# Optimization experiments

Measured on AMD Instinct MI355X. Metric: run time of the kernel, lower is better.

Reference implementation:

```python
import jax, jax.numpy as jnp
import numpy as np

N_NODES = 50000
N_EDGES = 800000
IN_FEATS = 128
HID = 64
HEADS = 3
NUM_CLASSES = 8
ATTN_SLOPE = 0.2   # DGL GATConv leaky_relu slope on attention logits
ACT_SLOPE = 0.01   # nn.LeakyReLU default


def setup_inputs() -> dict:
    key = jax.random.key(0)
    ks = jax.random.split(key, 40)
    inp = {}
    inp["x"] = jax.random.normal(ks[0], (N_NODES, IN_FEATS), dtype=jnp.float32)
    inp["src"] = jax.random.randint(ks[1], (N_EDGES,), 0, N_NODES)
    inp["dst"] = jax.random.randint(ks[2], (N_EDGES,), 0, N_NODES)
    dims_in = [IN_FEATS, HID, HID, HID, HID]
    i = 3
    for l, din in enumerate(dims_in, start=1):
        inp[f"W{l}"] = jax.random.normal(ks[i], (din, HEADS * HID), dtype=jnp.float32) / np.float32(np.sqrt(din)); i += 1
        inp[f"b{l}"] = jnp.zeros((HEADS * HID,), dtype=jnp.float32)
        inp[f"al{l}"] = jax.random.normal(ks[i], (HEADS, HID), dtype=jnp.float32) * 0.1; i += 1
        inp[f"ar{l}"] = jax.random.normal(ks[i], (HEADS, HID), dtype=jnp.float32) * 0.1; i += 1
    inp["Wo"] = jax.random.normal(ks[i], (HID, NUM_CLASSES), dtype=jnp.float32) / np.float32(np.sqrt(HID)); i += 1
    inp["bo"] = jnp.zeros((NUM_CLASSES,), dtype=jnp.float32)
    return inp


def _gatconv(h, W, b, al, ar, src, dst):
    # h: [N, din] -> feat: [N, H, F]
    feat = (h @ W).reshape(N_NODES, HEADS, HID)
    el = jnp.einsum('nhf,hf->nh', feat, al)   # [N, H]
    er = jnp.einsum('nhf,hf->nh', feat, ar)   # [N, H]
    e = jax.nn.leaky_relu(el[src] + er[dst], ATTN_SLOPE)        # [E, H]
    # numerically-stable edge softmax segmented by destination node
    m = jax.ops.segment_max(e, dst, num_segments=N_NODES)      # [N, H]
    ex = jnp.exp(e - m[dst])                                   # [E, H]
    denom = jax.ops.segment_sum(ex, dst, num_segments=N_NODES)  # [N, H]
    alpha = ex / denom[dst]                                    # [E, H]
    msg = alpha[:, :, None] * feat[src]                        # [E, H, F]
    out = jax.ops.segment_sum(msg, dst, num_segments=N_NODES)  # [N, H, F]
    return out + b.reshape(HEADS, HID)


def reference(x, src, dst,
              W1, b1, al1, ar1,
              W2, b2, al2, ar2,
              W3, b3, al3, ar3,
              W4, b4, al4, ar4,
              W5, b5, al5, ar5,
              Wo, bo):
    layers = [(W1, b1, al1, ar1), (W2, b2, al2, ar2), (W3, b3, al3, ar3),
              (W4, b4, al4, ar4), (W5, b5, al5, ar5)]
    h = x
    for (W, b, al, ar) in layers:
        h = jax.nn.leaky_relu(_gatconv(h, W, b, al, ar, src, dst), ACT_SLOPE)
        h = h.mean(axis=1)  # mean over heads -> [N, F]
    return h @ Wo + bo      # [N, num_classes]
```

## Files before the change

kernel.cpp:

```cpp
#include <hip/hip_runtime.h>
#include <hip/hip_fp16.h>
#include <cstdint>

#define N_NODES 50000
#define N_EDGES 800000
#define IN_FEATS 128
#define HID 64
#define HEADS 3
#define NUM_CLASSES 8
#define ATTN_SLOPE 0.2f
#define ACT_SLOPE 0.01f

__device__ __forceinline__ float lrelu(float x, float s) { return x > 0.f ? x : s * x; }

__global__ void k_deg(const int* __restrict__ dst, int* __restrict__ deg, int E) {
    int i = blockIdx.x * blockDim.x + threadIdx.x;
    if (i < E) atomicAdd(&deg[dst[i]], 1);
}

__global__ __launch_bounds__(256) void k_scan1(const int* __restrict__ deg, int* __restrict__ off,
                                               int* __restrict__ bsum, int n) {
    __shared__ int wtot[4];
    int tid = threadIdx.x;
    int lane = tid & 63, wid = tid >> 6;
    int base = blockIdx.x * 2048 + tid * 8;
    int v[8];
    if (base + 8 <= n) {
        int4 a = *(const int4*)&deg[base];
        int4 b = *(const int4*)&deg[base + 4];
        v[0] = a.x; v[1] = a.y; v[2] = a.z; v[3] = a.w;
        v[4] = b.x; v[5] = b.y; v[6] = b.z; v[7] = b.w;
    } else {
#pragma unroll
        for (int j = 0; j < 8; ++j) v[j] = (base + j < n) ? deg[base + j] : 0;
    }
    int s[8];
    s[0] = v[0];
#pragma unroll
    for (int j = 1; j < 8; ++j) s[j] = s[j - 1] + v[j];
    int t = s[7];
    int incl = t;
    for (int o = 1; o < 64; o <<= 1) {
        int u = __shfl_up(incl, o);
        if (lane >= o) incl += u;
    }
    int excl = incl - t;
    if (lane == 63) wtot[wid] = incl;
    __syncthreads();
    int wprefix = 0;
    for (int w = 0; w < wid; ++w) wprefix += wtot[w];
    int base_off = wprefix + excl;
#pragma unroll
    for (int j = 0; j < 8; ++j)
        if (base + j < n) off[base + j] = base_off + s[j] - v[j];
    if (tid == 0) bsum[blockIdx.x] = wtot[0] + wtot[1] + wtot[2] + wtot[3];
}

__global__ __launch_bounds__(64) void k_scan2(int* __restrict__ bsum, int nb) {
    int tid = threadIdx.x;
    int v = (tid < nb) ? bsum[tid] : 0;
    int incl = v;
    for (int o = 1; o < 64; o <<= 1) {
        int u = __shfl_up(incl, o);
        if (tid >= o) incl += u;
    }
    if (tid < nb) bsum[tid] = incl - v;
}

__global__ __launch_bounds__(256) void k_scan3(int* __restrict__ off, const int* __restrict__ bsum,
                                               int n, int E) {
    int i = blockIdx.x * blockDim.x + threadIdx.x;
    if (i < n) off[i] += bsum[i >> 11];
    if (i == 0) off[n] = E;
}

__global__ void k_fill(const int* __restrict__ src, const int* __restrict__ dst,
                       const int* __restrict__ off, int* __restrict__ cur,
                       int* __restrict__ ssrc, int E) {
    int i = blockIdx.x * blockDim.x + threadIdx.x;
    if (i < E) {
        int d = dst[i];
        int p = atomicAdd(&cur[d], 1);
        ssrc[off[d] + p] = src[i];
    }
}

__global__ __launch_bounds__(256) void k_gemm(const float* __restrict__ h, const float* __restrict__ W,
                                              const float* __restrict__ al, const float* __restrict__ ar,
                                              __half* __restrict__ feat,
                                              float* __restrict__ el, float* __restrict__ er,
                                              int N, int din) {
    __shared__ float Hl[128][68];
    __shared__ float Wl[64][64];
    int tid = threadIdx.x;
    int cg = tid & 15;
    int rg = tid >> 4;
    int row0 = blockIdx.x * 128;
    int head = blockIdx.y;
    int c0 = head * 64;

    float acc[8][4];
#pragma unroll
    for (int i = 0; i < 8; ++i)
#pragma unroll
        for (int c = 0; c < 4; ++c) acc[i][c] = 0.f;

    for (int k0 = 0; k0 < din; k0 += 64) {
        for (int j = tid; j < 1024; j += 256) {
            int k = j >> 4, c4 = (j & 15) << 2;
            *(float4*)&Wl[k][c4] = *(const float4*)&W[(size_t)(k0 + k) * 192 + c0 + c4];
        }
        for (int j = tid; j < 2048; j += 256) {
            int r = j >> 4, kk = (j & 15) << 2;
            int row = row0 + r;
            float4 v = make_float4(0.f, 0.f, 0.f, 0.f);
            if (row < N) v = *(const float4*)&h[(size_t)row * din + k0 + kk];
            *(float4*)&Hl[r][kk] = v;
        }
        __syncthreads();

        for (int k = 0; k < 64; k += 4) {
            float4 w0 = *(const float4*)&Wl[k + 0][cg << 2];
            float4 w1 = *(const float4*)&Wl[k + 1][cg << 2];
            float4 w2 = *(const float4*)&Wl[k + 2][cg << 2];
            float4 w3 = *(const float4*)&Wl[k + 3][cg << 2];
#pragma unroll
            for (int i = 0; i < 8; ++i) {
                float4 hv = *(const float4*)&Hl[rg + 16 * i][k];
                acc[i][0] += hv.x * w0.x + hv.y * w1.x + hv.z * w2.x + hv.w * w3.x;
                acc[i][1] += hv.x * w0.y + hv.y * w1.y + hv.z * w2.y + hv.w * w3.y;
                acc[i][2] += hv.x * w0.z + hv.y * w1.z + hv.z * w2.z + hv.w * w3.z;
                acc[i][3] += hv.x * w0.w + hv.y * w1.w + hv.z * w2.w + hv.w * w3.w;
            }
        }
        __syncthreads();
    }

    float alv0 = al[c0 + (cg << 2) + 0], alv1 = al[c0 + (cg << 2) + 1];
    float alv2 = al[c0 + (cg << 2) + 2], alv3 = al[c0 + (cg << 2) + 3];
    float arv0 = ar[c0 + (cg << 2) + 0], arv1 = ar[c0 + (cg << 2) + 1];
    float arv2 = ar[c0 + (cg << 2) + 2], arv3 = ar[c0 + (cg << 2) + 3];
#pragma unroll
    for (int i = 0; i < 8; ++i) {
        int row = row0 + rg + 16 * i;
        bool ok = (row < N);
        float4 a4 = make_float4(acc[i][0], acc[i][1], acc[i][2], acc[i][3]);
        if (ok) {
            union { __half2 h2[2]; uint2 u; } pk;
            pk.h2[0] = __floats2half2_rn(a4.x, a4.y);
            pk.h2[1] = __floats2half2_rn(a4.z, a4.w);
            *(uint2*)&feat[(size_t)row * 192 + c0 + (cg << 2)] = pk.u;
        }
        float pl = a4.x * alv0 + a4.y * alv1 + a4.z * alv2 + a4.w * alv3;
        float pr = a4.x * arv0 + a4.y * arv1 + a4.z * arv2 + a4.w * arv3;
        for (int o = 1; o < 16; o <<= 1) {
            pl += __shfl_xor(pl, o);
            pr += __shfl_xor(pr, o);
        }
        if (ok && cg == 0) {
            el[row * HEADS + head] = pl;
            er[row * HEADS + head] = pr;
        }
    }
}

__global__ __launch_bounds__(256) void k_agg(const int* __restrict__ off, const int* __restrict__ ssrc,
                                             const float* __restrict__ el, const float* __restrict__ er,
                                             const __half* __restrict__ feat, const float* __restrict__ b,
                                             float* __restrict__ hout, int N) {
    __shared__ float4 ebuf[4][64];
    int wib = threadIdx.x >> 6;
    int wid = (blockIdx.x * blockDim.x + threadIdx.x) >> 6;
    int lane = threadIdx.x & 63;
    if (wid >= N) return;
    int start = off[wid], end = off[wid + 1];
    int cnt = end - start;
    float er0 = er[wid * HEADS + 0];
    float er1 = er[wid * HEADS + 1];
    float er2 = er[wid * HEADS + 2];
    float acc0 = 0.f, acc1 = 0.f, acc2 = 0.f;
    float den0 = 0.f, den1 = 0.f, den2 = 0.f;

    if (cnt <= 64) {
        int s0 = 0;
        float ea = -3.4e38f, eb = -3.4e38f, ec = -3.4e38f;
        if (lane < cnt) {
            s0 = ssrc[start + lane];
            ea = lrelu(el[s0 * HEADS + 0] + er0, ATTN_SLOPE);
            eb = lrelu(el[s0 * HEADS + 1] + er1, ATTN_SLOPE);
            ec = lrelu(el[s0 * HEADS + 2] + er2, ATTN_SLOPE);
        }
        float ma = ea, mb = eb, mc = ec;
        for (int o = 32; o > 0; o >>= 1) {
            ma = fmaxf(ma, __shfl_xor(ma, o));
            mb = fmaxf(mb, __shfl_xor(mb, o));
            mc = fmaxf(mc, __shfl_xor(mc, o));
        }
        float xa = (lane < cnt) ? __expf(ea - ma) : 0.f;
        float xb = (lane < cnt) ? __expf(eb - mb) : 0.f;
        float xc = (lane < cnt) ? __expf(ec - mc) : 0.f;
        float da = xa, db = xb, dc = xc;
        for (int o = 32; o > 0; o >>= 1) {
            da += __shfl_xor(da, o);
            db += __shfl_xor(db, o);
            dc += __shfl_xor(dc, o);
        }
        den0 = da; den1 = db; den2 = dc;
        ebuf[wib][lane] = make_float4(__int_as_float(s0), xa, xb, xc);
        int t = 0;
        for (; t + 4 <= cnt; t += 4) {
            float4 v0 = ebuf[wib][t + 0];
            float4 v1 = ebuf[wib][t + 1];
            float4 v2 = ebuf[wib][t + 2];
            float4 v3 = ebuf[wib][t + 3];
            const __half* f0 = feat + (size_t)__float_as_int(v0.x) * 192 + lane;
            const __half* f1 = feat + (size_t)__float_as_int(v1.x) * 192 + lane;
            const __half* f2 = feat + (size_t)__float_as_int(v2.x) * 192 + lane;
            const __half* f3 = feat + (size_t)__float_as_int(v3.x) * 192 + lane;
            float p00 = __half2float(f0[0]), p01 = __half2float(f0[64]), p02 = __half2float(f0[128]);
            float p10 = __half2float(f1[0]), p11 = __half2float(f1[64]), p12 = __half2float(f1[128]);
            float p20 = __half2float(f2[0]), p21 = __half2float(f2[64]), p22 = __half2float(f2[128]);
            float p30 = __half2float(f3[0]), p31 = __half2float(f3[64]), p32 = __half2float(f3[128]);
            acc0 += v0.y * p00; acc1 += v0.z * p01; acc2 += v0.w * p02;
            acc0 += v1.y * p10; acc1 += v1.z * p11; acc2 += v1.w * p12;
            acc0 += v2.y * p20; acc1 += v2.z * p21; acc2 += v2.w * p22;
            acc0 += v3.y * p30; acc1 += v3.z * p31; acc2 += v3.w * p32;
        }
        for (; t < cnt; ++t) {
            float4 v = ebuf[wib][t];
            const __half* fr = feat + (size_t)__float_as_int(v.x) * 192 + lane;
            acc0 += v.y * __half2float(fr[0]);
            acc1 += v.z * __half2float(fr[64]);
            acc2 += v.w * __half2float(fr[128]);
        }
    } else {
        float ma = -3.4e38f, mb = -3.4e38f, mc = -3.4e38f;
        for (int j = start + lane; j < end; j += 64) {
            int s = ssrc[j];
            ma = fmaxf(ma, lrelu(el[s * HEADS + 0] + er0, ATTN_SLOPE));
            mb = fmaxf(mb, lrelu(el[s * HEADS + 1] + er1, ATTN_SLOPE));
            mc = fmaxf(mc, lrelu(el[s * HEADS + 2] + er2, ATTN_SLOPE));
        }
        for (int o = 32; o > 0; o >>= 1) {
            ma = fmaxf(ma, __shfl_xor(ma, o));
            mb = fmaxf(mb, __shfl_xor(mb, o));
            mc = fmaxf(mc, __shfl_xor(mc, o));
        }
        float da = 0.f, db = 0.f, dc = 0.f;
        for (int j0 = start; j0 < end; j0 += 64) {
            int jj = j0 + lane;
            int s0 = 0;
            float xa = 0.f, xb = 0.f, xc = 0.f;
            if (jj < end) {
                s0 = ssrc[jj];
                xa = __expf(lrelu(el[s0 * HEADS + 0] + er0, ATTN_SLOPE) - ma);
                xb = __expf(lrelu(el[s0 * HEADS + 1] + er1, ATTN_SLOPE) - mb);
                xc = __expf(lrelu(el[s0 * HEADS + 2] + er2, ATTN_SLOPE) - mc);
            }
            da += xa; db += xb; dc += xc;
            ebuf[wib][lane] = make_float4(__int_as_float(s0), xa, xb, xc);
            int c = min(64, end - j0);
            int t = 0;
            for (; t + 4 <= c; t += 4) {
                float4 v0 = ebuf[wib][t + 0];
                float4 v1 = ebuf[wib][t + 1];
                float4 v2 = ebuf[wib][t + 2];
                float4 v3 = ebuf[wib][t + 3];
                const __half* f0 = feat + (size_t)__float_as_int(v0.x) * 192 + lane;
                const __half* f1 = feat + (size_t)__float_as_int(v1.x) * 192 + lane;
                const __half* f2 = feat + (size_t)__float_as_int(v2.x) * 192 + lane;
                const __half* f3 = feat + (size_t)__float_as_int(v3.x) * 192 + lane;
                float p00 = __half2float(f0[0]), p01 = __half2float(f0[64]), p02 = __half2float(f0[128]);
                float p10 = __half2float(f1[0]), p11 = __half2float(f1[64]), p12 = __half2float(f1[128]);
                float p20 = __half2float(f2[0]), p21 = __half2float(f2[64]), p22 = __half2float(f2[128]);
                float p30 = __half2float(f3[0]), p31 = __half2float(f3[64]), p32 = __half2float(f3[128]);
                acc0 += v0.y * p00; acc1 += v0.z * p01; acc2 += v0.w * p02;
                acc0 += v1.y * p10; acc1 += v1.z * p11; acc2 += v1.w * p12;
                acc0 += v2.y * p20; acc1 += v2.z * p21; acc2 += v2.w * p22;
                acc0 += v3.y * p30; acc1 += v3.z * p31; acc2 += v3.w * p32;
            }
            for (; t < c; ++t) {
                float4 v = ebuf[wib][t];
                const __half* fr = feat + (size_t)__float_as_int(v.x) * 192 + lane;
                acc0 += v.y * __half2float(fr[0]);
                acc1 += v.z * __half2float(fr[64]);
                acc2 += v.w * __half2float(fr[128]);
            }
        }
        for (int o = 32; o > 0; o >>= 1) {
            da += __shfl_xor(da, o);
            db += __shfl_xor(db, o);
            dc += __shfl_xor(dc, o);
        }
        den0 = da; den1 = db; den2 = dc;
    }

    float v0 = (cnt > 0) ? acc0 / den0 : 0.f;
    float v1 = (cnt > 0) ? acc1 / den1 : 0.f;
    float v2 = (cnt > 0) ? acc2 / den2 : 0.f;
    float hsum = lrelu(v0 + b[lane], ACT_SLOPE)
               + lrelu(v1 + b[64 + lane], ACT_SLOPE)
               + lrelu(v2 + b[128 + lane], ACT_SLOPE);
    hout[wid * 64 + lane] = hsum * (1.f / 3.f);
}

__global__ __launch_bounds__(256) void k_out(const float* __restrict__ h, const float* __restrict__ Wo,
                                             const float* __restrict__ bo, float* __restrict__ out, int N) {
    __shared__ float Hl[32][65];
    __shared__ float Wl[64 * 8];
    int tid = threadIdx.x;
    int n0 = blockIdx.x * 32;
    for (int i = tid; i < 32 * 64; i += 256) {
        int r = i >> 6, k = i & 63;
        Hl[r][k] = (n0 + r < N) ? h[(n0 + r) * 64 + k] : 0.f;
    }
    for (int i = tid; i < 512; i += 256) Wl[i] = Wo[i];
    __syncthreads();
    int r = tid >> 3, c = tid & 7;
    float acc = 0.f;
    for (int k = 0; k < 64; ++k) acc += Hl[r][k] * Wl[k * 8 + c];
    int row = n0 + r;
    if (row < N) out[row * 8 + c] = acc + bo[c];
}

extern "C" void kernel_launch(void* const* d_in, const int* in_sizes, int n_in,
                              void* d_out, int out_size, void* d_ws, size_t ws_size,
                              hipStream_t stream) {
    const float* x  = (const float*)d_in[0];
    const int* src  = (const int*)d_in[1];
    const int* dst  = (const int*)d_in[2];
    const float *W[5], *b[5], *al[5], *ar[5];
    for (int l = 0; l < 5; ++l) {
        W[l]  = (const float*)d_in[3 + l * 4];
        b[l]  = (const float*)d_in[4 + l * 4];
        al[l] = (const float*)d_in[5 + l * 4];
        ar[l] = (const float*)d_in[6 + l * 4];
    }
    const float* Wo = (const float*)d_in[23];
    const float* bo = (const float*)d_in[24];
    float* out = (float*)d_out;

    char* ws = (char*)d_ws;
    auto alloc = [&](size_t bytes) {
        char* p = ws;
        ws += (bytes + 255) & ~size_t(255);
        return p;
    };
    __half* feat = (__half*)alloc(sizeof(__half) * (size_t)N_NODES * 192);
    float* el   = (float*)alloc(sizeof(float) * (size_t)N_NODES * HEADS);
    float* er   = (float*)alloc(sizeof(float) * (size_t)N_NODES * HEADS);
    float* h0   = (float*)alloc(sizeof(float) * (size_t)N_NODES * 64);
    float* h1   = (float*)alloc(sizeof(float) * (size_t)N_NODES * 64);
    int* deg    = (int*)alloc(sizeof(int) * N_NODES);
    int* off    = (int*)alloc(sizeof(int) * (N_NODES + 1));
    int* cur    = (int*)alloc(sizeof(int) * N_NODES);
    int* ssrc   = (int*)alloc(sizeof(int) * N_EDGES);
    int* bsum   = (int*)alloc(sizeof(int) * 64);

    const int NB = (N_NODES + 2047) / 2048;
    hipMemsetAsync(deg, 0, sizeof(int) * N_NODES, stream);
    hipMemsetAsync(cur, 0, sizeof(int) * N_NODES, stream);
    k_deg<<<(N_EDGES + 255) / 256, 256, 0, stream>>>(dst, deg, N_EDGES);
    k_scan1<<<NB, 256, 0, stream>>>(deg, off, bsum, N_NODES);
    k_scan2<<<1, 64, 0, stream>>>(bsum, NB);
    k_scan3<<<(N_NODES + 255) / 256, 256, 0, stream>>>(off, bsum, N_NODES, N_EDGES);
    k_fill<<<(N_EDGES + 255) / 256, 256, 0, stream>>>(src, dst, off, cur, ssrc, N_EDGES);

    const float* hin = x;
    float* hbuf[2] = {h0, h1};
    int din = IN_FEATS;
    for (int l = 0; l < 5; ++l) {
        dim3 ggrid((N_NODES + 127) / 128, HEADS);
        k_gemm<<<ggrid, 256, 0, stream>>>(hin, W[l], al[l], ar[l], feat, el, er, N_NODES, din);
        float* hn = hbuf[l & 1];
        k_agg<<<(N_NODES * 64 + 255) / 256, 256, 0, stream>>>(off, ssrc, el, er, feat, b[l], hn, N_NODES);
        hin = hn;
        din = HID;
    }
    k_out<<<(N_NODES + 31) / 32, 256, 0, stream>>>(hin, Wo, bo, out, N_NODES);
}
```

Baseline: 624.1 us.

## Use fp16 MFMA for per-layer GEMM and store hidden activations in fp16

Replaces the fp32 scalar-FMA GEMM with MFMA 16x16x32 fp16 instructions. The input x and the weights are pre-cast to fp16 (weights transposed) in two new kernels. Hidden activations between layers are now stored as fp16, which halves GEMM input bandwidth. In exchange it adds two cast kernels, uses uncoalesced scalar half stores for feat in the epilogue, and lowers precision of the activations.

```diff
diff --git a/kernel.cpp b/kernel.cpp
--- a/kernel.cpp
+++ b/kernel.cpp
@@ -10,6 +10,9 @@
 #define NUM_CLASSES 8
 #define ATTN_SLOPE 0.2f
 #define ACT_SLOPE 0.01f
+
+typedef _Float16 half8 __attribute__((ext_vector_type(8)));
+typedef float f32x4 __attribute__((ext_vector_type(4)));
 
 __device__ __forceinline__ float lrelu(float x, float s) { return x > 0.f ? x : s * x; }
 
@@ -85,81 +88,118 @@
     }
 }
 
-__global__ __launch_bounds__(256) void k_gemm(const float* __restrict__ h, const float* __restrict__ W,
+__global__ __launch_bounds__(256) void k_xcast(const float* __restrict__ x, _Float16* __restrict__ xh, int n8) {
+    int i = blockIdx.x * blockDim.x + threadIdx.x;
+    if (i < n8) {
+        float4 a = *(const float4*)&x[i * 8];
+        float4 b = *(const float4*)&x[i * 8 + 4];
+        _Float16 v[8] = {(_Float16)a.x, (_Float16)a.y, (_Float16)a.z, (_Float16)a.w,
+                         (_Float16)b.x, (_Float16)b.y, (_Float16)b.z, (_Float16)b.w};
+        *(uint4*)&xh[i * 8] = *(uint4*)v;
+    }
+}
+
+__global__ __launch_bounds__(256) void k_wcast(const float* __restrict__ W1, const float* __restrict__ W2,
+                                               const float* __restrict__ W3, const float* __restrict__ W4,
+                                               const float* __restrict__ W5, _Float16* __restrict__ Wt) {
+    int i = blockIdx.x * blockDim.x + threadIdx.x;
+    if (i >= 24576 + 4 * 12288) return;
+    const float* W; int din; int idx; _Float16* out;
+    if (i < 24576) { W = W1; din = 128; idx = i; out = Wt; }
+    else {
+        int j = i - 24576; int l = j / 12288; idx = j % 12288;
+        W = (l == 0) ? W2 : (l == 1) ? W3 : (l == 2) ? W4 : W5;
+        din = 64;
+        out = Wt + 24576 + l * 12288;
+    }
+    int col = idx / din, k = idx % din;
+    out[idx] = (_Float16)W[k * 192 + col];
+}
+
+__global__ __launch_bounds__(256) void k_gemm(const _Float16* __restrict__ h, const _Float16* __restrict__ Wt,
                                               const float* __restrict__ al, const float* __restrict__ ar,
-                                              __half* __restrict__ feat,
+                                              _Float16* __restrict__ feat,
                                               float* __restrict__ el, float* __restrict__ er,
                                               int N, int din) {
-    __shared__ float Hl[128][68];
-    __shared__ float Wl[64][64];
+    __shared__ __align__(16) _Float16 Hl[128 * 136];
+    __shared__ __align__(16) _Float16 Wl[64 * 136];
+    const int K = din;
+    const int LD = K + 8;
+    const int KC = K >> 3;
     int tid = threadIdx.x;
-    int cg = tid & 15;
-    int rg = tid >> 4;
     int row0 = blockIdx.x * 128;
     int head = blockIdx.y;
     int c0 = head * 64;
 
-    float acc[8][4];
-#pragma unroll
-    for (int i = 0; i < 8; ++i)
-#pragma unroll
-        for (int c = 0; c < 4; ++c) acc[i][c] = 0.f;
-
-    for (int k0 = 0; k0 < din; k0 += 64) {
-        for (int j = tid; j < 1024; j += 256) {
-            int k = j >> 4, c4 = (j & 15) << 2;
-            *(float4*)&Wl[k][c4] = *(const float4*)&W[(size_t)(k0 + k) * 192 + c0 + c4];
-        }
-        for (int j = tid; j < 2048; j += 256) {
-            int r = j >> 4, kk = (j & 15) << 2;
-            int row = row0 + r;
-            float4 v = make_float4(0.f, 0.f, 0.f, 0.f);
-            if (row < N) v = *(const float4*)&h[(size_t)row * din + k0 + kk];
-            *(float4*)&Hl[r][kk] = v;
-        }
-        __syncthreads();
-
-        for (int k = 0; k < 64; k += 4) {
-            float4 w0 = *(const float4*)&Wl[k + 0][cg << 2];
-            float4 w1 = *(const float4*)&Wl[k + 1][cg << 2];
-            float4 w2 = *(const float4*)&Wl[k + 2][cg << 2];
-            float4 w3 = *(const float4*)&Wl[k + 3][cg << 2];
-#pragma unroll
-            for (int i = 0; i < 8; ++i) {
-                float4 hv = *(const float4*)&Hl[rg + 16 * i][k];
-                acc[i][0] += hv.x * w0.x + hv.y * w1.x + hv.z * w2.x + hv.w * w3.x;
-                acc[i][1] += hv.x * w0.y + hv.y * w1.y + hv.z * w2.y + hv.w * w3.y;
-                acc[i][2] += hv.x * w0.z + hv.y * w1.z + hv.z * w2.z + hv.w * w3.z;
-                acc[i][3] += hv.x * w0.w + hv.y * w1.w + hv.z * w2.w + hv.w * w3.w;
-            }
-        }
-        __syncthreads();
-    }
-
-    float alv0 = al[c0 + (cg << 2) + 0], alv1 = al[c0 + (cg << 2) + 1];
-    float alv2 = al[c0 + (cg << 2) + 2], alv3 = al[c0 + (cg << 2) + 3];
-    float arv0 = ar[c0 + (cg << 2) + 0], arv1 = ar[c0 + (cg << 2) + 1];
-    float arv2 = ar[c0 + (cg << 2) + 2], arv3 = ar[c0 + (cg << 2) + 3];
-#pragma unroll
-    for (int i = 0; i < 8; ++i) {
-        int row = row0 + rg + 16 * i;
-        bool ok = (row < N);
-        float4 a4 = make_float4(acc[i][0], acc[i][1], acc[i][2], acc[i][3]);
-        if (ok) {
-            union { __half2 h2[2]; uint2 u; } pk;
-            pk.h2[0] = __floats2half2_rn(a4.x, a4.y);
-            pk.h2[1] = __floats2half2_rn(a4.z, a4.w);
-            *(uint2*)&feat[(size_t)row * 192 + c0 + (cg << 2)] = pk.u;
-        }
-        float pl = a4.x * alv0 + a4.y * alv1 + a4.z * alv2 + a4.w * alv3;
-        float pr = a4.x * arv0 + a4.y * arv1 + a4.z * arv2 + a4.w * arv3;
-        for (int o = 1; o < 16; o <<= 1) {
-            pl += __shfl_xor(pl, o);
-            pr += __shfl_xor(pr, o);
-        }
-        if (ok && cg == 0) {
-            el[row * HEADS + head] = pl;
-            er[row * HEADS + head] = pr;
+    for (int i = tid; i < 64 * KC; i += 256) {
+        int col = i / KC, c8 = i % KC;
+        *(uint4*)&Wl[col * LD + c8 * 8] = *(const uint4*)&Wt[(size_t)(c0 + col) * K + c8 * 8];
+    }
+    for (int i = tid; i < 128 * KC; i += 256) {
+        int r = i / KC, c8 = i % KC;
+        int row = row0 + r;
+        uint4 v = make_uint4(0, 0, 0, 0);
+        if (row < N) v = *(const uint4*)&h[(size_t)row * K + c8 * 8];
+        *(uint4*)&Hl[r * LD + c8 * 8] = v;
+    }
+    __syncthreads();
+
+    int wid = tid >> 6, lane = tid & 63;
+    int l15 = lane & 15;
+    int koff = (lane >> 4) * 8;
+    int wr0 = wid * 32;
+
+    f32x4 acc[2][4] = {};
+    int nkb = K >> 5;
+    for (int kb = 0; kb < nkb; ++kb) {
+        int kbase = kb * 32 + koff;
+        half8 a0 = *(half8*)&Hl[(wr0 + l15) * LD + kbase];
+        half8 a1 = *(half8*)&Hl[(wr0 + 16 + l15) * LD + kbase];
+        half8 b0 = *(half8*)&Wl[(l15) * LD + kbase];
+        half8 b1 = *(half8*)&Wl[(16 + l15) * LD + kbase];
+        half8 b2 = *(half8*)&Wl[(32 + l15) * LD + kbase];
+        half8 b3 = *(half8*)&Wl[(48 + l15) * LD + kbase];
+        acc[0][0] = __builtin_amdgcn_mfma_f32_16x16x32_f16(a0, b0, acc[0][0], 0, 0, 0);
+        acc[0][1] = __builtin_amdgcn_mfma_f32_16x16x32_f16(a0, b1, acc[0][1], 0, 0, 0);
+        acc[0][2] = __builtin_amdgcn_mfma_f32_16x16x32_f16(a0, b2, acc[0][2], 0, 0, 0);
+        acc[0][3] = __builtin_amdgcn_mfma_f32_16x16x32_f16(a0, b3, acc[0][3], 0, 0, 0);
+        acc[1][0] = __builtin_amdgcn_mfma_f32_16x16x32_f16(a1, b0, acc[1][0], 0, 0, 0);
+        acc[1][1] = __builtin_amdgcn_mfma_f32_16x16x32_f16(a1, b1, acc[1][1], 0, 0, 0);
+        acc[1][2] = __builtin_amdgcn_mfma_f32_16x16x32_f16(a1, b2, acc[1][2], 0, 0, 0);
+        acc[1][3] = __builtin_amdgcn_mfma_f32_16x16x32_f16(a1, b3, acc[1][3], 0, 0, 0);
+    }
+
+    float alv[4], arv[4];
+#pragma unroll
+    for (int ct = 0; ct < 4; ++ct) {
+        alv[ct] = al[c0 + ct * 16 + l15];
+        arv[ct] = ar[c0 + ct * 16 + l15];
+    }
+
+#pragma unroll
+    for (int rt = 0; rt < 2; ++rt) {
+#pragma unroll
+        for (int r = 0; r < 4; ++r) {
+            int row = row0 + wr0 + rt * 16 + (lane >> 4) * 4 + r;
+            bool ok = (row < N);
+            float c0v = acc[rt][0][r], c1v = acc[rt][1][r], c2v = acc[rt][2][r], c3v = acc[rt][3][r];
+            if (ok) {
+                size_t base = (size_t)row * 192 + c0;
+                feat[base + l15]      = (_Float16)c0v;
+                feat[base + 16 + l15] = (_Float16)c1v;
+                feat[base + 32 + l15] = (_Float16)c2v;
+                feat[base + 48 + l15] = (_Float16)c3v;
+            }
+            float pl = c0v * alv[0] + c1v * alv[1] + c2v * alv[2] + c3v * alv[3];
+            float pr = c0v * arv[0] + c1v * arv[1] + c2v * arv[2] + c3v * arv[3];
+            for (int o = 1; o < 16; o <<= 1) {
+                pl += __shfl_xor(pl, o);
+                pr += __shfl_xor(pr, o);
+            }
+            if (ok && l15 == 0) {
+                el[row * HEADS + head] = pl;
+                er[row * HEADS + head] = pr;
+            }
         }
     }
 }
@@ -167,7 +207,7 @@
 __global__ __launch_bounds__(256) void k_agg(const int* __restrict__ off, const int* __restrict__ ssrc,
                                              const float* __restrict__ el, const float* __restrict__ er,
                                              const __half* __restrict__ feat, const float* __restrict__ b,
-                                             float* __restrict__ hout, int N) {
+                                             __half* __restrict__ hout, int N) {
     __shared__ float4 ebuf[4][64];
     int wib = threadIdx.x >> 6;
     int wid = (blockIdx.x * blockDim.x + threadIdx.x) >> 6;
@@ -301,10 +341,10 @@
     float hsum = lrelu(v0 + b[lane], ACT_SLOPE)
                + lrelu(v1 + b[64 + lane], ACT_SLOPE)
                + lrelu(v2 + b[128 + lane], ACT_SLOPE);
-    hout[wid * 64 + lane] = hsum * (1.f / 3.f);
-}
-
-__global__ __launch_bounds__(256) void k_out(const float* __restrict__ h, const float* __restrict__ Wo,
+    hout[wid * 64 + lane] = __float2half(hsum * (1.f / 3.f));
+}
+
+__global__ __launch_bounds__(256) void k_out(const __half* __restrict__ h, const float* __restrict__ Wo,
                                              const float* __restrict__ bo, float* __restrict__ out, int N) {
     __shared__ float Hl[32][65];
     __shared__ float Wl[64 * 8];
@@ -312,7 +352,7 @@
     int n0 = blockIdx.x * 32;
     for (int i = tid; i < 32 * 64; i += 256) {
         int r = i >> 6, k = i & 63;
-        Hl[r][k] = (n0 + r < N) ? h[(n0 + r) * 64 + k] : 0.f;
+        Hl[r][k] = (n0 + r < N) ? __half2float(h[(n0 + r) * 64 + k]) : 0.f;
     }
     for (int i = tid; i < 512; i += 256) Wl[i] = Wo[i];
     __syncthreads();
@@ -346,11 +386,13 @@
         ws += (bytes + 255) & ~size_t(255);
         return p;
     };
-    __half* feat = (__half*)alloc(sizeof(__half) * (size_t)N_NODES * 192);
-    float* el   = (float*)alloc(sizeof(float) * (size_t)N_NODES * HEADS);
-    float* er   = (float*)alloc(sizeof(float) * (size_t)N_NODES * HEADS);
-    float* h0   = (float*)alloc(sizeof(float) * (size_t)N_NODES * 64);
-    float* h1   = (float*)alloc(sizeof(float) * (size_t)N_NODES * 64);
+    _Float16* feat = (_Float16*)alloc(sizeof(_Float16) * (size_t)N_NODES * 192);
+    float* el      = (float*)alloc(sizeof(float) * (size_t)N_NODES * HEADS);
+    float* er      = (float*)alloc(sizeof(float) * (size_t)N_NODES * HEADS);
+    _Float16* xh   = (_Float16*)alloc(sizeof(_Float16) * (size_t)N_NODES * IN_FEATS);
+    _Float16* h0   = (_Float16*)alloc(sizeof(_Float16) * (size_t)N_NODES * 64);
+    _Float16* h1   = (_Float16*)alloc(sizeof(_Float16) * (size_t)N_NODES * 64);
+    _Float16* wt   = (_Float16*)alloc(sizeof(_Float16) * (24576 + 4 * 12288));
     int* deg    = (int*)alloc(sizeof(int) * N_NODES);
     int* off    = (int*)alloc(sizeof(int) * (N_NODES + 1));
     int* cur    = (int*)alloc(sizeof(int) * N_NODES);
@@ -358,24 +400,29 @@
     int* bsum   = (int*)alloc(sizeof(int) * 64);
 
     const int NB = (N_NODES + 2047) / 2048;
-    hipMemsetAsync(deg, 0, sizeof(int) * N_NODES, stream);
-    hipMemsetAsync(cur, 0, sizeof(int) * N_NODES, stream);
+    (void)hipMemsetAsync(deg, 0, sizeof(int) * N_NODES, stream);
+    (void)hipMemsetAsync(cur, 0, sizeof(int) * N_NODES, stream);
     k_deg<<<(N_EDGES + 255) / 256, 256, 0, stream>>>(dst, deg, N_EDGES);
     k_scan1<<<NB, 256, 0, stream>>>(deg, off, bsum, N_NODES);
     k_scan2<<<1, 64, 0, stream>>>(bsum, NB);
     k_scan3<<<(N_NODES + 255) / 256, 256, 0, stream>>>(off, bsum, N_NODES, N_EDGES);
     k_fill<<<(N_EDGES + 255) / 256, 256, 0, stream>>>(src, dst, off, cur, ssrc, N_EDGES);
-
-    const float* hin = x;
-    float* hbuf[2] = {h0, h1};
+    k_xcast<<<(N_NODES * IN_FEATS / 8 + 255) / 256, 256, 0, stream>>>(x, xh, N_NODES * IN_FEATS / 8);
+    k_wcast<<<(24576 + 4 * 12288 + 255) / 256, 256, 0, stream>>>(W[0], W[1], W[2], W[3], W[4], wt);
+
+    const _Float16* hin = xh;
+    _Float16* hbuf[2] = {h0, h1};
+    const _Float16* wts[5] = {wt, wt + 24576, wt + 24576 + 12288, wt + 24576 + 2 * 12288, wt + 24576 + 3 * 12288};
     int din = IN_FEATS;
     for (int l = 0; l < 5; ++l) {
         dim3 ggrid((N_NODES + 127) / 128, HEADS);
-        k_gemm<<<ggrid, 256, 0, stream>>>(hin, W[l], al[l], ar[l], feat, el, er, N_NODES, din);
-        float* hn = hbuf[l & 1];
-        k_agg<<<(N_NODES * 64 + 255) / 256, 256, 0, stream>>>(off, ssrc, el, er, feat, b[l], hn, N_NODES);
+        k_gemm<<<ggrid, 256, 0, stream>>>(hin, wts[l], al[l], ar[l], feat, el, er, N_NODES, din);
+        _Float16* hn = hbuf[l & 1];
+        k_agg<<<(N_NODES * 64 + 255) / 256, 256, 0, stream>>>(off, ssrc, el, er,
+                                                              (const __half*)feat, b[l],
+                                                              (__half*)hn, N_NODES);
         hin = hn;
         din = HID;
     }
-    k_out<<<(N_NODES + 31) / 32, 256, 0, stream>>>(hin, Wo, bo, out, N_NODES);
-}
+    k_out<<<(N_NODES + 31) / 32, 256, 0, stream>>>((const __half*)hin, Wo, bo, out, N_NODES);
+}
```

After: 537.0 us. -14.0%, faster.
